# Kernel tuning notes

Hardware: AMD Instinct MI355X
Metric: run time of the kernel (lower is better)

Reference implementation:

```python
import jax, jax.numpy as jnp
import numpy as np

# Norse LIFParameters defaults (method='super', alpha=100)
DT = 1e-3
TAU_SYN_INV = 200.0   # 1 / 5e-3
TAU_MEM_INV = 100.0   # 1 / 1e-2
V_TH = 1.0
V_LEAK = 0.0
V_RESET = 0.0
ALPHA = 100.0

@jax.custom_vjp
def superspike(x):
    return (x > 0).astype(x.dtype)

def _ss_fwd(x):
    return superspike(x), x

def _ss_bwd(x, g):
    return (g / (ALPHA * jnp.abs(x) + 1.0) ** 2,)

superspike.defvjp(_ss_fwd, _ss_bwd)

T, B, F, H1, OUT = 100, 512, 784, 1024, 10

def setup_inputs() -> dict:
    key = jax.random.key(0)
    k1, k2, k3 = jax.random.split(key, 3)
    x = jax.random.normal(k1, (T, B, F), jnp.float32)
    # fc0: Linear(784, h1) with bias
    W0 = jax.random.normal(k2, (H1, F), jnp.float32) / np.sqrt(F)
    b0 = jnp.zeros((H1,), jnp.float32)
    # LILinearCell input_weights: Linear(h1, 10) without bias
    Wout = jax.random.normal(k3, (OUT, H1), jnp.float32) / np.sqrt(H1)
    return {"x": x, "W0": W0, "b0": b0, "Wout": Wout}

def reference(x, W0, b0, Wout):
    Tn, Bn, Fn = x.shape
    H = W0.shape[0]
    O = Wout.shape[0]

    def step(state, xt):
        v_lif, i_lif, v_li, i_li = state
        z_in = xt @ W0.T + b0                                    # [B, H]
        # LIF cell step
        v_dec = v_lif + DT * TAU_MEM_INV * ((V_LEAK - v_lif) + i_lif)
        i_dec = i_lif * (1.0 - DT * TAU_SYN_INV)
        z = superspike(v_dec - V_TH)                             # spikes [B, H]
        v_new = (1.0 - z) * v_dec + z * V_RESET
        i_new = i_dec + z_in
        # LI linear cell step (voltage output)
        v_li_new = v_li + DT * TAU_MEM_INV * ((V_LEAK - v_li) + i_li)
        i_li_new = i_li * (1.0 - DT * TAU_SYN_INV) + z @ Wout.T  # [B, O]
        return (v_new, i_new, v_li_new, i_li_new), v_li_new

    z0 = lambda s: jnp.zeros(s, x.dtype)
    init = (z0((Bn, H)), z0((Bn, H)), z0((Bn, O)), z0((Bn, O)))
    _, voltages = jax.lax.scan(step, init, x)
    return voltages  # [T, B, 10]
```

## Files before the change

### kernel.cpp

```cpp
#include <hip/hip_runtime.h>

#define T_TOT 100
#define BATCH 512
#define FIN   784
#define HID   1024
#define NOUT  10
#define KP    800
#define BK    32
#define KSTEPS 25

typedef _Float16 f16x8 __attribute__((ext_vector_type(8)));
typedef float    f32x4 __attribute__((ext_vector_type(4)));

#define AS1C(p) ((const __attribute__((address_space(1))) void*)(p))
#define AS3(p)  ((__attribute__((address_space(3))) void*)(p))

__global__ __launch_bounds__(256)
void cvt_split(const float* __restrict__ src, _Float16* __restrict__ hi,
               _Float16* __restrict__ lo, int nrows)
{
    int idx = blockIdx.x * 256 + threadIdx.x;
    if (idx >= nrows * 100) return;
    int row = idx / 100;
    int k0  = (idx - row * 100) * 8;
    f16x8 h, l;
    if (k0 < FIN) {
        float4 a = *(const float4*)(src + (size_t)row * FIN + k0);
        float4 b = *(const float4*)(src + (size_t)row * FIN + k0 + 4);
        float xs[8] = {a.x, a.y, a.z, a.w, b.x, b.y, b.z, b.w};
        #pragma unroll
        for (int j = 0; j < 8; ++j) {
            _Float16 hh = (_Float16)xs[j];
            h[j] = hh;
            l[j] = (_Float16)((xs[j] - (float)hh) * 4096.0f);
        }
    } else {
        #pragma unroll
        for (int j = 0; j < 8; ++j) { h[j] = (_Float16)0.f; l[j] = (_Float16)0.f; }
    }
    *(f16x8*)(hi + (size_t)row * KP + k0) = h;
    *(f16x8*)(lo + (size_t)row * KP + k0) = l;
}

__global__ __launch_bounds__(256, 2)
void gemm_mfma(const _Float16* __restrict__ Xhi, const _Float16* __restrict__ Xlo,
               const _Float16* __restrict__ Whi, const _Float16* __restrict__ Wlo,
               const float* __restrict__ bias, float* __restrict__ Z, int mb)
{
    __shared__ char smem[65536];
    const int tid  = threadIdx.x;
    const int lane = tid & 63;
    const int wid  = tid >> 6;
    const int wm   = wid >> 1;
    const int wn   = wid & 1;
    const int fr   = lane & 15;
    const int fg   = lane >> 4;

    const int j = blockIdx.x;
    int bm, bn;
    if ((mb & 7) == 0) {
        bm = (j & 7) | ((j >> 6) << 3);
        bn = (j >> 3) & 7;
    } else {
        bm = j >> 3;
        bn = j & 7;
    }
    const size_t row0 = (size_t)bm * 128;
    const int    col0 = bn * 128;

    f32x4 accm[4][4], accc[4][4];
    #pragma unroll
    for (int a = 0; a < 4; ++a)
        #pragma unroll
        for (int b = 0; b < 4; ++b) {
            accm[a][b] = (f32x4){0.f, 0.f, 0.f, 0.f};
            accc[a][b] = (f32x4){0.f, 0.f, 0.f, 0.f};
        }

    auto stage = [&](int buf, int kt) {
        const int kof = kt * BK;
        #pragma unroll
        for (int q = 0; q < 2; ++q) {
            const int lin = q * 256 + tid;
            const int row = lin >> 2;
            const int pos = lin & 3;
            const int gg  = pos ^ ((row >> 1) & 3);
            const int ldsw = buf * 32768 + q * 4096 + wid * 1024;
            const size_t ga = (row0 + row) * (size_t)KP + kof + gg * 8;
            const size_t gb = (size_t)(col0 + row) * KP + kof + gg * 8;
            __builtin_amdgcn_global_load_lds(AS1C(Xhi + ga), AS3(smem + ldsw),         16, 0, 0);
            __builtin_amdgcn_global_load_lds(AS1C(Xlo + ga), AS3(smem + ldsw +  8192), 16, 0, 0);
            __builtin_amdgcn_global_load_lds(AS1C(Whi + gb), AS3(smem + ldsw + 16384), 16, 0, 0);
            __builtin_amdgcn_global_load_lds(AS1C(Wlo + gb), AS3(smem + ldsw + 24576), 16, 0, 0);
        }
    };

    auto compute = [&](int buf) {
        const char* base = smem + buf * 32768;
        f16x8 ah[4], al[4], bh[4], bl[4];
        #pragma unroll
        for (int mf = 0; mf < 4; ++mf) {
            const int row = wm * 64 + mf * 16 + fr;
            const int off = row * 64 + ((fg ^ ((row >> 1) & 3)) << 4);
            ah[mf] = *(const f16x8*)(base + off);
            al[mf] = *(const f16x8*)(base + 8192 + off);
        }
        #pragma unroll
        for (int nf = 0; nf < 4; ++nf) {
            const int row = wn * 64 + nf * 16 + fr;
            const int off = row * 64 + ((fg ^ ((row >> 1) & 3)) << 4);
            bh[nf] = *(const f16x8*)(base + 16384 + off);
            bl[nf] = *(const f16x8*)(base + 24576 + off);
        }
        #pragma unroll
        for (int mf = 0; mf < 4; ++mf)
            #pragma unroll
            for (int nf = 0; nf < 4; ++nf) {
                accm[mf][nf] = __builtin_amdgcn_mfma_f32_16x16x32_f16(ah[mf], bh[nf], accm[mf][nf], 0, 0, 0);
                accc[mf][nf] = __builtin_amdgcn_mfma_f32_16x16x32_f16(ah[mf], bl[nf], accc[mf][nf], 0, 0, 0);
                accc[mf][nf] = __builtin_amdgcn_mfma_f32_16x16x32_f16(al[mf], bh[nf], accc[mf][nf], 0, 0, 0);
            }
    };

    stage(0, 0);
    int buf = 0;
    for (int kt = 0; kt < KSTEPS; ++kt) {
        __syncthreads();
        if (kt + 1 < KSTEPS) stage(buf ^ 1, kt + 1);
        compute(buf);
        buf ^= 1;
    }

    #pragma unroll
    for (int nf = 0; nf < 4; ++nf) {
        const int colg = col0 + wn * 64 + nf * 16 + fr;
        const float bv = bias[colg];
        #pragma unroll
        for (int mf = 0; mf < 4; ++mf) {
            const size_t rowg = row0 + wm * 64 + mf * 16 + fg * 4;
            #pragma unroll
            for (int i = 0; i < 4; ++i)
                Z[(rowg + i) * HID + colg] =
                    accm[mf][nf][i] + accc[mf][nf][i] * 2.44140625e-4f + bv;
        }
    }
}

__global__ __launch_bounds__(256, 2)
void lif_scan(const float* __restrict__ Z, const float* __restrict__ Wout,
              float* __restrict__ out,
              float* __restrict__ st_v, float* __restrict__ st_i,
              float* __restrict__ st_vli, float* __restrict__ st_ili,
              int t0, int tn, int first, int last)
{
#pragma clang fp contract(off)
    __shared__ float Wlds[NOUT][HID];
    __shared__ float red[2][4][NOUT];

    const int tid  = threadIdx.x;
    const int b    = blockIdx.x;
    const int h4   = tid * 4;
    const int lane = tid & 63;
    const int wv   = tid >> 6;

    #pragma unroll
    for (int o = 0; o < NOUT; ++o)
        *(float4*)&Wlds[o][h4] = *(const float4*)&Wout[o * HID + h4];

    float v[4], cu[4];
    if (first) {
        #pragma unroll
        for (int j = 0; j < 4; ++j) { v[j] = 0.f; cu[j] = 0.f; }
    } else {
        float4 tv = *(const float4*)&st_v[(size_t)b*HID + h4];
        float4 ti = *(const float4*)&st_i[(size_t)b*HID + h4];
        v[0]=tv.x; v[1]=tv.y; v[2]=tv.z; v[3]=tv.w;
        cu[0]=ti.x; cu[1]=ti.y; cu[2]=ti.z; cu[3]=ti.w;
    }
    float vli = 0.f, ili = 0.f;
    if (!first && tid < NOUT) {
        vli = st_vli[b*NOUT + tid];
        ili = st_ili[b*NOUT + tid];
    }

    __syncthreads();

    const float* Zb = Z + (size_t)b * HID + h4;
    float4 zn = *(const float4*)Zb;

    for (int t = 0; t < tn; ++t) {
        float4 zc = zn;
        if (t + 1 < tn) zn = *(const float4*)(Zb + (size_t)(t+1) * BATCH * HID);

        const float za[4] = {zc.x, zc.y, zc.z, zc.w};
        float zf[4];
        bool anyz = false;
        #pragma unroll
        for (int j = 0; j < 4; ++j) {
            float tmp  = (0.0f - v[j]) + cu[j];
            float vdec = v[j] + 0.1f * tmp;
            bool  z    = vdec > 1.0f;
            zf[j] = z ? 1.0f : 0.0f;
            anyz  = anyz || z;
            v[j]  = z ? 0.0f : vdec;
            cu[j] = cu[j] * 0.8f + za[j];
        }

        float p[NOUT];
        #pragma unroll
        for (int o = 0; o < NOUT; ++o) p[o] = 0.f;

        if (__any(anyz)) {
            if (anyz) {
                #pragma unroll
                for (int o = 0; o < NOUT; ++o) {
                    float4 w = *(const float4*)&Wlds[o][h4];
                    p[o] = zf[0]*w.x + zf[1]*w.y + zf[2]*w.z + zf[3]*w.w;
                }
            }
            #pragma unroll
            for (int o = 0; o < NOUT; ++o) {
                float s = p[o];
                s += __shfl_xor(s, 1);
                s += __shfl_xor(s, 2);
                s += __shfl_xor(s, 4);
                s += __shfl_xor(s, 8);
                s += __shfl_xor(s, 16);
                s += __shfl_xor(s, 32);
                p[o] = s;
            }
        }

        const int par = t & 1;
        if (lane == 0) {
            #pragma unroll
            for (int o = 0; o < NOUT; ++o) red[par][wv][o] = p[o];
        }
        __syncthreads();
        if (tid < NOUT) {
            float s = red[par][0][tid] + red[par][1][tid]
                    + red[par][2][tid] + red[par][3][tid];
            float tmp  = (0.0f - vli) + ili;
            float vnew = vli + 0.1f * tmp;
            ili = ili * 0.8f + s;
            vli = vnew;
            out[((size_t)(t0 + t) * BATCH + b) * NOUT + tid] = vnew;
        }
    }

    if (!last) {
        *(float4*)&st_v[(size_t)b*HID + h4] = make_float4(v[0], v[1], v[2], v[3]);
        *(float4*)&st_i[(size_t)b*HID + h4] = make_float4(cu[0], cu[1], cu[2], cu[3]);
        if (tid < NOUT) { st_vli[b*NOUT + tid] = vli; st_ili[b*NOUT + tid] = ili; }
    }
}

extern "C" void kernel_launch(void* const* d_in, const int* in_sizes, int n_in,
                              void* d_out, int out_size, void* d_ws, size_t ws_size,
                              hipStream_t stream)
{
    const float* x    = (const float*)d_in[0];
    const float* W0   = (const float*)d_in[1];
    const float* b0   = (const float*)d_in[2];
    const float* Wout = (const float*)d_in[3];
    float* out = (float*)d_out;

    char* ws = (char*)d_ws;
    float* st_v   = (float*)ws;
    float* st_i   = st_v   + (size_t)BATCH * HID;
    float* st_vli = st_i   + (size_t)BATCH * HID;
    float* st_ili = st_vli + BATCH * NOUT;
    _Float16* Whi = (_Float16*)(st_ili + BATCH * NOUT);
    _Float16* Wlo = Whi + (size_t)HID * KP;
    char* dyn = (char*)(Wlo + (size_t)HID * KP);

    const size_t fixed = (size_t)(dyn - ws);
    const size_t per_t = (size_t)BATCH * HID * 4
                       + (size_t)BATCH * KP * 2 * 2;
    size_t avail = (ws_size > fixed) ? ws_size - fixed : 0;
    int tch = (int)(avail / per_t);
    if (tch > T_TOT) tch = T_TOT;
    if (tch >= 2) tch &= ~1;
    if (tch < 1) tch = 1;

    float*    Zbuf = (float*)dyn;
    _Float16* Xhi  = (_Float16*)(dyn + (size_t)tch * BATCH * HID * 4);
    _Float16* Xlo  = Xhi + (size_t)tch * BATCH * KP;

    hipLaunchKernelGGL(cvt_split, dim3((HID * 100 + 255) / 256), dim3(256), 0, stream,
                       W0, Whi, Wlo, HID);

    for (int t0 = 0; t0 < T_TOT; t0 += tch) {
        const int tn    = (T_TOT - t0 < tch) ? (T_TOT - t0) : tch;
        const int nrows = tn * BATCH;
        const int mb    = nrows / 128;

        hipLaunchKernelGGL(cvt_split, dim3((nrows * 100 + 255) / 256), dim3(256), 0, stream,
                           x + (size_t)t0 * BATCH * FIN, Xhi, Xlo, nrows);
        hipLaunchKernelGGL(gemm_mfma, dim3(mb * 8), dim3(256), 0, stream,
                           Xhi, Xlo, Whi, Wlo, b0, Zbuf, mb);
        hipLaunchKernelGGL(lif_scan, dim3(BATCH), dim3(256), 0, stream,
                           Zbuf, Wout, out, st_v, st_i, st_vli, st_ili,
                           t0, tn, (t0 == 0) ? 1 : 0, (t0 + tn >= T_TOT) ? 1 : 0);
    }
}
```

Baseline: 537.4 us.

## Split LI readout into separate kernel to remove per-step block barriers in LIF scan

```diff
diff --git a/kernel.cpp b/kernel.cpp
--- a/kernel.cpp
+++ b/kernel.cpp
@@ -8,6 +8,7 @@
 #define KP    800
 #define BK    32
 #define KSTEPS 25
+#define NGRP  16
 
 typedef _Float16 f16x8 __attribute__((ext_vector_type(8)));
 typedef float    f32x4 __attribute__((ext_vector_type(4)));
@@ -146,64 +147,74 @@
     }
 }
 
+__device__ __forceinline__ float dpp_sum16(float v)
+{
+    int x;
+    x = __builtin_amdgcn_update_dpp(0, __builtin_bit_cast(int, v), 0xB1, 0xF, 0xF, true);
+    v += __builtin_bit_cast(float, x);
+    x = __builtin_amdgcn_update_dpp(0, __builtin_bit_cast(int, v), 0x4E, 0xF, 0xF, true);
+    v += __builtin_bit_cast(float, x);
+    x = __builtin_amdgcn_update_dpp(0, __builtin_bit_cast(int, v), 0x141, 0xF, 0xF, true);
+    v += __builtin_bit_cast(float, x);
+    x = __builtin_amdgcn_update_dpp(0, __builtin_bit_cast(int, v), 0x140, 0xF, 0xF, true);
+    v += __builtin_bit_cast(float, x);
+    return v;
+}
+
 __global__ __launch_bounds__(256, 2)
 void lif_scan(const float* __restrict__ Z, const float* __restrict__ Wout,
-              float* __restrict__ out,
+              float* __restrict__ S,
               float* __restrict__ st_v, float* __restrict__ st_i,
-              float* __restrict__ st_vli, float* __restrict__ st_ili,
-              int t0, int tn, int first, int last)
+              int tn, int first, int last)
 {
 #pragma clang fp contract(off)
-    __shared__ float Wlds[NOUT][HID];
-    __shared__ float red[2][4][NOUT];
-
-    const int tid  = threadIdx.x;
-    const int b    = blockIdx.x;
-    const int h4   = tid * 4;
-    const int lane = tid & 63;
-    const int wv   = tid >> 6;
-
+    const int tid   = threadIdx.x;
+    const int b     = blockIdx.x;
+    const int lane  = tid & 63;
+    const int w     = tid >> 6;
+    const int hglob = w * 256 + lane * 4;
+
+    float wreg[NOUT][4];
     #pragma unroll
-    for (int o = 0; o < NOUT; ++o)
-        *(float4*)&Wlds[o][h4] = *(const float4*)&Wout[o * HID + h4];
+    for (int o = 0; o < NOUT; ++o) {
+        float4 t4 = *(const float4*)&Wout[o * HID + hglob];
+        wreg[o][0] = t4.x; wreg[o][1] = t4.y; wreg[o][2] = t4.z; wreg[o][3] = t4.w;
+    }
 
     float v[4], cu[4];
     if (first) {
         #pragma unroll
-        for (int j = 0; j < 4; ++j) { v[j] = 0.f; cu[j] = 0.f; }
+        for (int jj = 0; jj < 4; ++jj) { v[jj] = 0.f; cu[jj] = 0.f; }
     } else {
-        float4 tv = *(const float4*)&st_v[(size_t)b*HID + h4];
-        float4 ti = *(const float4*)&st_i[(size_t)b*HID + h4];
+        float4 tv = *(const float4*)&st_v[(size_t)b * HID + hglob];
+        float4 ti = *(const float4*)&st_i[(size_t)b * HID + hglob];
         v[0]=tv.x; v[1]=tv.y; v[2]=tv.z; v[3]=tv.w;
         cu[0]=ti.x; cu[1]=ti.y; cu[2]=ti.z; cu[3]=ti.w;
     }
-    float vli = 0.f, ili = 0.f;
-    if (!first && tid < NOUT) {
-        vli = st_vli[b*NOUT + tid];
-        ili = st_ili[b*NOUT + tid];
-    }
-
-    __syncthreads();
-
-    const float* Zb = Z + (size_t)b * HID + h4;
-    float4 zn = *(const float4*)Zb;
+
+    const float* Zb = Z + (size_t)b * HID + hglob;
+    float4 z0 = *(const float4*)Zb;
+    float4 z1 = (tn > 1) ? *(const float4*)(Zb + (size_t)BATCH * HID)     : z0;
+    float4 z2 = (tn > 2) ? *(const float4*)(Zb + (size_t)2 * BATCH * HID) : z1;
+
+    const int g = w * 4 + (lane >> 4);
 
     for (int t = 0; t < tn; ++t) {
-        float4 zc = zn;
-        if (t + 1 < tn) zn = *(const float4*)(Zb + (size_t)(t+1) * BATCH * HID);
+        float4 zc = z0; z0 = z1; z1 = z2;
+        if (t + 3 < tn) z2 = *(const float4*)(Zb + (size_t)(t + 3) * BATCH * HID);
 
         const float za[4] = {zc.x, zc.y, zc.z, zc.w};
         float zf[4];
         bool anyz = false;
         #pragma unroll
-        for (int j = 0; j < 4; ++j) {
-            float tmp  = (0.0f - v[j]) + cu[j];
-            float vdec = v[j] + 0.1f * tmp;
+        for (int jj = 0; jj < 4; ++jj) {
+            float tmp  = (0.0f - v[jj]) + cu[jj];
+            float vdec = v[jj] + 0.1f * tmp;
             bool  z    = vdec > 1.0f;
-            zf[j] = z ? 1.0f : 0.0f;
-            anyz  = anyz || z;
-            v[j]  = z ? 0.0f : vdec;
-            cu[j] = cu[j] * 0.8f + za[j];
+            zf[jj] = z ? 1.0f : 0.0f;
+            anyz   = anyz || z;
+            v[jj]  = z ? 0.0f : vdec;
+            cu[jj] = cu[jj] * 0.8f + za[jj];
         }
 
         float p[NOUT];
@@ -213,46 +224,54 @@
         if (__any(anyz)) {
             if (anyz) {
                 #pragma unroll
-                for (int o = 0; o < NOUT; ++o) {
-                    float4 w = *(const float4*)&Wlds[o][h4];
-                    p[o] = zf[0]*w.x + zf[1]*w.y + zf[2]*w.z + zf[3]*w.w;
-                }
+                for (int o = 0; o < NOUT; ++o)
+                    p[o] = zf[0]*wreg[o][0] + zf[1]*wreg[o][1]
+                         + zf[2]*wreg[o][2] + zf[3]*wreg[o][3];
             }
             #pragma unroll
-            for (int o = 0; o < NOUT; ++o) {
-                float s = p[o];
-                s += __shfl_xor(s, 1);
-                s += __shfl_xor(s, 2);
-                s += __shfl_xor(s, 4);
-                s += __shfl_xor(s, 8);
-                s += __shfl_xor(s, 16);
-                s += __shfl_xor(s, 32);
-                p[o] = s;
-            }
-        }
-
-        const int par = t & 1;
-        if (lane == 0) {
+            for (int o = 0; o < NOUT; ++o) p[o] = dpp_sum16(p[o]);
+        }
+
+        if ((lane & 15) == 0) {
+            float* sp = S + ((size_t)t * BATCH + b) * (NGRP * NOUT) + g * NOUT;
             #pragma unroll
-            for (int o = 0; o < NOUT; ++o) red[par][wv][o] = p[o];
-        }
-        __syncthreads();
-        if (tid < NOUT) {
-            float s = red[par][0][tid] + red[par][1][tid]
-                    + red[par][2][tid] + red[par][3][tid];
-            float tmp  = (0.0f - vli) + ili;
-            float vnew = vli + 0.1f * tmp;
-            ili = ili * 0.8f + s;
-            vli = vnew;
-            out[((size_t)(t0 + t) * BATCH + b) * NOUT + tid] = vnew;
+            for (int o = 0; o < NOUT; ++o) sp[o] = p[o];
         }
     }
 
     if (!last) {
-        *(float4*)&st_v[(size_t)b*HID + h4] = make_float4(v[0], v[1], v[2], v[3]);
-        *(float4*)&st_i[(size_t)b*HID + h4] = make_float4(cu[0], cu[1], cu[2], cu[3]);
-        if (tid < NOUT) { st_vli[b*NOUT + tid] = vli; st_ili[b*NOUT + tid] = ili; }
-    }
+        *(float4*)&st_v[(size_t)b * HID + hglob] = make_float4(v[0], v[1], v[2], v[3]);
+        *(float4*)&st_i[(size_t)b * HID + hglob] = make_float4(cu[0], cu[1], cu[2], cu[3]);
+    }
+}
+
+__global__ __launch_bounds__(256)
+void li_scan(const float* __restrict__ S, float* __restrict__ out,
+             float* __restrict__ st_vli, float* __restrict__ st_ili,
+             int t0, int tn, int first, int last)
+{
+#pragma clang fp contract(off)
+    const int id = blockIdx.x * 256 + threadIdx.x;
+    if (id >= BATCH * NOUT) return;
+    const int b = id / NOUT;
+    const int o = id - b * NOUT;
+
+    float vli = 0.f, ili = 0.f;
+    if (!first) { vli = st_vli[id]; ili = st_ili[id]; }
+
+    const float* Sp = S + (size_t)b * (NGRP * NOUT) + o;
+    for (int t = 0; t < tn; ++t) {
+        const float* p = Sp + (size_t)t * BATCH * (NGRP * NOUT);
+        float s = 0.f;
+        #pragma unroll
+        for (int gg = 0; gg < NGRP; ++gg) s += p[gg * NOUT];
+        float tmp  = (0.0f - vli) + ili;
+        float vnew = vli + 0.1f * tmp;
+        ili = ili * 0.8f + s;
+        vli = vnew;
+        out[((size_t)(t0 + t) * BATCH + b) * NOUT + o] = vnew;
+    }
+    if (!last) { st_vli[id] = vli; st_ili[id] = ili; }
 }
 
 extern "C" void kernel_launch(void* const* d_in, const int* in_sizes, int n_in,
@@ -276,7 +295,8 @@
 
     const size_t fixed = (size_t)(dyn - ws);
     const size_t per_t = (size_t)BATCH * HID * 4
-                       + (size_t)BATCH * KP * 2 * 2;
+                       + (size_t)BATCH * KP * 2 * 2
+                       + (size_t)BATCH * NGRP * NOUT * 4;
     size_t avail = (ws_size > fixed) ? ws_size - fixed : 0;
     int tch = (int)(avail / per_t);
     if (tch > T_TOT) tch = T_TOT;
@@ -286,6 +306,7 @@
     float*    Zbuf = (float*)dyn;
     _Float16* Xhi  = (_Float16*)(dyn + (size_t)tch * BATCH * HID * 4);
     _Float16* Xlo  = Xhi + (size_t)tch * BATCH * KP;
+    float*    Sbuf = (float*)(Xlo + (size_t)tch * BATCH * KP);
 
     hipLaunchKernelGGL(cvt_split, dim3((HID * 100 + 255) / 256), dim3(256), 0, stream,
                        W0, Whi, Wlo, HID);
@@ -300,7 +321,10 @@
         hipLaunchKernelGGL(gemm_mfma, dim3(mb * 8), dim3(256), 0, stream,
                            Xhi, Xlo, Whi, Wlo, b0, Zbuf, mb);
         hipLaunchKernelGGL(lif_scan, dim3(BATCH), dim3(256), 0, stream,
-                           Zbuf, Wout, out, st_v, st_i, st_vli, st_ili,
+                           Zbuf, Wout, Sbuf, st_v, st_i,
+                           tn, (t0 == 0) ? 1 : 0, (t0 + tn >= T_TOT) ? 1 : 0);
+        hipLaunchKernelGGL(li_scan, dim3((BATCH * NOUT + 255) / 256), dim3(256), 0, stream,
+                           Sbuf, out, st_vli, st_ili,
                            t0, tn, (t0 == 0) ? 1 : 0, (t0 + tn >= T_TOT) ? 1 : 0);
     }
 }
```

Measured after the change: 525.7 us. 2.2% less time.
